# Kernel optimization log

Hardware: AMD Instinct MI355X
Metric: run time of the kernel (lower is better)

The kernel has to match this reference:

```python
import jax, jax.numpy as jnp
import numpy as np

EPS = 1e-6
ENERGY_THRESHOLD = 0.95
LS_INIT = 1e-5


def setup_inputs() -> dict:
    key = jax.random.key(0)
    k_x, k_u, k_s, k_v = jax.random.split(key, 4)
    dim, max_rank = 4096, 16
    x = jax.random.normal(k_x, (4, 2048, dim), dtype=jnp.float32)
    U = jax.random.normal(k_u, (dim, max_rank), dtype=jnp.float32) * 0.02
    S = jax.random.uniform(k_s, (max_rank,), dtype=jnp.float32)
    V = jax.random.normal(k_v, (max_rank, dim), dtype=jnp.float32) * 0.02
    norm_weight = jnp.ones((dim,), dtype=jnp.float32)
    gamma = jnp.full((dim,), LS_INIT, dtype=jnp.float32)
    return {"x": x, "U": U, "S": S, "V": V,
            "norm_weight": norm_weight, "gamma": gamma}


def _rank_mask(S):
    # Effective rank from singular-value energy (non-differentiable decision,
    # matching torch's .item() host sync which detaches it from autograd).
    s_abs = jnp.abs(S)
    cum = jnp.cumsum(s_abs) / jnp.maximum(s_abs.sum(), 1e-8)
    hit = cum >= ENERGY_THRESHOLD
    r = jnp.where(hit.any(), jnp.argmax(hit) + 1, S.shape[0])
    keep = (jnp.arange(S.shape[0]) < r).astype(S.dtype)
    return jax.lax.stop_gradient(keep)


def reference(x, U, S, V, norm_weight, gamma):
    # RMSNorm (computed in fp32, matching x.float() in torch)
    xf = x.astype(jnp.float32)
    x_norm = (xf * jax.lax.rsqrt(jnp.mean(xf * xf, axis=-1, keepdims=True) + EPS)).astype(x.dtype)
    x_norm = x_norm * norm_weight
    # Adaptive-rank low-rank projection: masking columns >= r equals slicing [:r]
    keep = _rank_mask(S)
    h = jnp.einsum('bsd,dr->bsr', x_norm, U)        # [B,S,max_rank]
    h = h * (S * keep)                               # zero out ranks >= r
    h = jnp.einsum('bsr,rd->bsd', h, V)             # [B,S,dim]
    # LayerScale + residual
    return x + h * gamma
```

## Files before the change

kernel.cpp:

```cpp
#include <hip/hip_runtime.h>

#define DIM   4096
#define RANK  16
#define ROWS  4
#define NT    512
#define NWAVE 8

typedef int   int2v  __attribute__((ext_vector_type(2)));
typedef float f32x4v __attribute__((ext_vector_type(4)));

__device__ __forceinline__ float f4get(const float4& v, int j) {
    switch (j) { case 0: return v.x; case 1: return v.y; case 2: return v.z; default: return v.w; }
}

__global__ __launch_bounds__(256) void transpose_U(const float* __restrict__ U,
                                                   float* __restrict__ Ut) {
    const int d = blockIdx.x * 256 + threadIdx.x;
    const float4* U4 = (const float4*)U;
    float4 u0 = U4[(size_t)d * 4 + 0];
    float4 u1 = U4[(size_t)d * 4 + 1];
    float4 u2 = U4[(size_t)d * 4 + 2];
    float4 u3 = U4[(size_t)d * 4 + 3];
    Ut[ 0*DIM + d] = u0.x; Ut[ 1*DIM + d] = u0.y; Ut[ 2*DIM + d] = u0.z; Ut[ 3*DIM + d] = u0.w;
    Ut[ 4*DIM + d] = u1.x; Ut[ 5*DIM + d] = u1.y; Ut[ 6*DIM + d] = u1.z; Ut[ 7*DIM + d] = u1.w;
    Ut[ 8*DIM + d] = u2.x; Ut[ 9*DIM + d] = u2.y; Ut[10*DIM + d] = u2.z; Ut[11*DIM + d] = u2.w;
    Ut[12*DIM + d] = u3.x; Ut[13*DIM + d] = u3.y; Ut[14*DIM + d] = u3.z; Ut[15*DIM + d] = u3.w;
}

__global__ __launch_bounds__(NT, 2) void arl_fused(
    const float* __restrict__ x,  const float* __restrict__ Ut,
    const float* __restrict__ S,  const float* __restrict__ V,
    const float* __restrict__ nw, const float* __restrict__ gamma,
    float* __restrict__ out)
{
    const int t    = threadIdx.x;
    const int w    = t >> 6;
    const int lane = t & 63;
    const int rg   = w & 3;
    const int dh   = w >> 2;
    const size_t row0 = (size_t)blockIdx.x * ROWS;

    const float4* x4   = (const float4*)(x + row0 * DIM);
    float4*       out4 = (float4*)(out + row0 * DIM);
    const float4* Ut4  = (const float4*)Ut;
    const float4* V4   = (const float4*)V;
    const float4* nw4  = (const float4*)nw;
    const float4* g4   = (const float4*)gamma;

    __shared__ __align__(16) float4 x_lds4[ROWS * (DIM/4)];
    __shared__ float s_ssq[NWAVE][ROWS];
    __shared__ float s_hraw[NWAVE][16];
    __shared__ __align__(16) float s_h[ROWS * RANK];

    #pragma unroll
    for (int i = 0; i < 8; ++i) {
        const int idx = i * NT + t;
        f32x4v val = __builtin_nontemporal_load((const f32x4v*)(x4 + idx));
        *(f32x4v*)&x_lds4[idx] = val;
    }
    __syncthreads();

    float v[16];
    #pragma unroll
    for (int i = 0; i < 16; ++i) v[i] = 0.f;
    float ssq[ROWS] = {0.f, 0.f, 0.f, 0.f};

    #pragma unroll 1
    for (int k = 0; k < 8; ++k) {
        const int d4 = dh * 512 + k * 64 + lane;
        const float4 wv = nw4[d4];
        float4 u[4];
        #pragma unroll
        for (int ql = 0; ql < 4; ++ql)
            u[ql] = Ut4[(size_t)(rg * 4 + ql) * (DIM/4) + d4];
        float4 xr[ROWS];
        #pragma unroll
        for (int r = 0; r < ROWS; ++r) xr[r] = x_lds4[r * (DIM/4) + d4];
        #pragma unroll
        for (int j = 0; j < 4; ++j) {
            const float wj = f4get(wv, j);
            float xn[ROWS];
            #pragma unroll
            for (int r = 0; r < ROWS; ++r) {
                const float xj = f4get(xr[r], j);
                ssq[r] = fmaf(xj, xj, ssq[r]);
                xn[r] = xj * wj;
            }
            #pragma unroll
            for (int ql = 0; ql < 4; ++ql) {
                const float uj = f4get(u[ql], j);
                #pragma unroll
                for (int r = 0; r < ROWS; ++r)
                    v[r*4+ql] = fmaf(xn[r], uj, v[r*4+ql]);
            }
        }
    }

    #pragma unroll
    for (int r = 0; r < ROWS; ++r) {
        float s = ssq[r];
        #pragma unroll
        for (int off = 32; off >= 1; off >>= 1) s += __shfl_xor(s, off, 64);
        if (lane == 0) s_ssq[w][r] = s;
    }

    #pragma unroll
    for (int i = 0; i < 8; ++i) {
        int a = __float_as_int(v[2*i]);
        int b = __float_as_int(v[2*i+1]);
        int2v pr = __builtin_amdgcn_permlane32_swap(a, b, false, false);
        v[i] = __int_as_float(pr.x) + __int_as_float(pr.y);
    }
    #pragma unroll
    for (int s = 1; s <= 3; ++s) {
        const int off = 32 >> s;
        const int n   = 8 >> s;
        const bool hi = (lane >> (5 - s)) & 1;
        #pragma unroll
        for (int i = 0; i < n; ++i) {
            float lo = v[2*i], hg = v[2*i+1];
            float slo = __shfl_xor(lo, off, 64);
            float shg = __shfl_xor(hg, off, 64);
            v[i] = hi ? (hg + shg) : (lo + slo);
        }
    }
    v[0] += __shfl_xor(v[0], 2, 64);
    v[0] += __shfl_xor(v[0], 1, 64);
    {
        const int idx = ((lane >> 5) & 1) | (((lane >> 4) & 1) << 1)
                      | (((lane >> 3) & 1) << 2) | (((lane >> 2) & 1) << 3);
        if ((lane & 3) == 0) s_hraw[w][idx] = v[0];
    }
    __syncthreads();

    if (t < 64) {
        const int r = t >> 4, q = t & 15;
        const int qg = q >> 2, ql = q & 3;
        const float hs = s_hraw[qg][r * 4 + ql] + s_hraw[qg + 4][r * 4 + ql];
        const float tot_ssq = s_ssq[0][r] + s_ssq[4][r];
        const float rstd = rsqrtf(tot_ssq * (1.0f / DIM) + 1e-6f);
        float tot = 0.f;
        #pragma unroll
        for (int i = 0; i < RANK; ++i) tot += fabsf(S[i]);
        const float denom = fmaxf(tot, 1e-8f);
        float cum = 0.f, se = 0.f;
        #pragma unroll
        for (int i = 0; i < RANK; ++i) {
            if (i == q) se = ((cum / denom) < 0.95f) ? S[i] : 0.f;
            cum += fabsf(S[i]);
        }
        s_h[t] = hs * se * rstd;
    }
    __syncthreads();

    const float4* s_h4 = (const float4*)s_h;
    #pragma unroll 1
    for (int k = 0; k < 2; ++k) {
        const int c = k * NT + t;
        float4 acc[ROWS];
        #pragma unroll
        for (int r = 0; r < ROWS; ++r) acc[r] = make_float4(0.f, 0.f, 0.f, 0.f);
        #pragma unroll 1
        for (int qg = 0; qg < 4; ++qg) {
            float4 vv[4];
            #pragma unroll
            for (int ql = 0; ql < 4; ++ql)
                vv[ql] = V4[(size_t)(qg*4 + ql) * (DIM/4) + c];
            #pragma unroll
            for (int r = 0; r < ROWS; ++r) {
                const float4 hq = s_h4[r * 4 + qg];
                #pragma unroll
                for (int ql = 0; ql < 4; ++ql) {
                    const float hqq = f4get(hq, ql);
                    acc[r].x = fmaf(hqq, vv[ql].x, acc[r].x);
                    acc[r].y = fmaf(hqq, vv[ql].y, acc[r].y);
                    acc[r].z = fmaf(hqq, vv[ql].z, acc[r].z);
                    acc[r].w = fmaf(hqq, vv[ql].w, acc[r].w);
                }
            }
        }
        const float4 g = g4[c];
        #pragma unroll
        for (int r = 0; r < ROWS; ++r) {
            const float4 xrr = x_lds4[r * (DIM/4) + c];
            float4 o;
            o.x = fmaf(g.x, acc[r].x, xrr.x);
            o.y = fmaf(g.y, acc[r].y, xrr.y);
            o.z = fmaf(g.z, acc[r].z, xrr.z);
            o.w = fmaf(g.w, acc[r].w, xrr.w);
            __builtin_nontemporal_store(*(const f32x4v*)&o,
                                        (f32x4v*)(out4 + (size_t)r * (DIM/4) + c));
        }
    }
}

extern "C" void kernel_launch(void* const* d_in, const int* in_sizes, int n_in,
                              void* d_out, int out_size, void* d_ws, size_t ws_size,
                              hipStream_t stream) {
    (void)in_sizes; (void)n_in; (void)ws_size;
    const float* x  = (const float*)d_in[0];
    const float* U  = (const float*)d_in[1];
    const float* S  = (const float*)d_in[2];
    const float* V  = (const float*)d_in[3];
    const float* nw = (const float*)d_in[4];
    const float* g  = (const float*)d_in[5];
    float* out = (float*)d_out;
    float* Ut  = (float*)d_ws;

    hipLaunchKernelGGL(transpose_U, dim3(DIM / 256), dim3(256), 0, stream, U, Ut);

    const int rows = out_size / DIM;
    const int grid = rows / ROWS;
    hipLaunchKernelGGL(arl_fused, dim3(grid), dim3(NT), 0, stream,
                       x, Ut, S, V, nw, g, out);
}
```

Measured before the change: 88.84 us.

## Drop LDS staging of x, fold norm weight into U, raise occupancy

Removes the 64KB shared-memory staging of the four x rows and reads x directly from global memory in both phases, relying on cache for the second read. Folds norm_weight into the transposed U in the prep kernel, which removes a load and a multiply per element in the main loop. Raises the launch-bounds occupancy hint from 2 to 8 blocks, which the smaller LDS footprint now allows. The risk is that x is re-read from global memory in the epilogue, and that the tighter register budget causes spills.

```diff
diff --git a/kernel.cpp b/kernel.cpp
--- a/kernel.cpp
+++ b/kernel.cpp
@@ -14,24 +14,25 @@
 }
 
 __global__ __launch_bounds__(256) void transpose_U(const float* __restrict__ U,
+                                                   const float* __restrict__ nw,
                                                    float* __restrict__ Ut) {
     const int d = blockIdx.x * 256 + threadIdx.x;
+    const float wv = nw[d];
     const float4* U4 = (const float4*)U;
     float4 u0 = U4[(size_t)d * 4 + 0];
     float4 u1 = U4[(size_t)d * 4 + 1];
     float4 u2 = U4[(size_t)d * 4 + 2];
     float4 u3 = U4[(size_t)d * 4 + 3];
-    Ut[ 0*DIM + d] = u0.x; Ut[ 1*DIM + d] = u0.y; Ut[ 2*DIM + d] = u0.z; Ut[ 3*DIM + d] = u0.w;
-    Ut[ 4*DIM + d] = u1.x; Ut[ 5*DIM + d] = u1.y; Ut[ 6*DIM + d] = u1.z; Ut[ 7*DIM + d] = u1.w;
-    Ut[ 8*DIM + d] = u2.x; Ut[ 9*DIM + d] = u2.y; Ut[10*DIM + d] = u2.z; Ut[11*DIM + d] = u2.w;
-    Ut[12*DIM + d] = u3.x; Ut[13*DIM + d] = u3.y; Ut[14*DIM + d] = u3.z; Ut[15*DIM + d] = u3.w;
-}
-
-__global__ __launch_bounds__(NT, 2) void arl_fused(
+    Ut[ 0*DIM + d] = u0.x*wv; Ut[ 1*DIM + d] = u0.y*wv; Ut[ 2*DIM + d] = u0.z*wv; Ut[ 3*DIM + d] = u0.w*wv;
+    Ut[ 4*DIM + d] = u1.x*wv; Ut[ 5*DIM + d] = u1.y*wv; Ut[ 6*DIM + d] = u1.z*wv; Ut[ 7*DIM + d] = u1.w*wv;
+    Ut[ 8*DIM + d] = u2.x*wv; Ut[ 9*DIM + d] = u2.y*wv; Ut[10*DIM + d] = u2.z*wv; Ut[11*DIM + d] = u2.w*wv;
+    Ut[12*DIM + d] = u3.x*wv; Ut[13*DIM + d] = u3.y*wv; Ut[14*DIM + d] = u3.z*wv; Ut[15*DIM + d] = u3.w*wv;
+}
+
+__global__ __launch_bounds__(NT, 8) void arl_fused(
     const float* __restrict__ x,  const float* __restrict__ Ut,
     const float* __restrict__ S,  const float* __restrict__ V,
-    const float* __restrict__ nw, const float* __restrict__ gamma,
-    float* __restrict__ out)
+    const float* __restrict__ gamma, float* __restrict__ out)
 {
     const int t    = threadIdx.x;
     const int w    = t >> 6;
@@ -44,22 +45,12 @@
     float4*       out4 = (float4*)(out + row0 * DIM);
     const float4* Ut4  = (const float4*)Ut;
     const float4* V4   = (const float4*)V;
-    const float4* nw4  = (const float4*)nw;
     const float4* g4   = (const float4*)gamma;
 
-    __shared__ __align__(16) float4 x_lds4[ROWS * (DIM/4)];
     __shared__ float s_ssq[NWAVE][ROWS];
     __shared__ float s_hraw[NWAVE][16];
     __shared__ __align__(16) float s_h[ROWS * RANK];
 
-    #pragma unroll
-    for (int i = 0; i < 8; ++i) {
-        const int idx = i * NT + t;
-        f32x4v val = __builtin_nontemporal_load((const f32x4v*)(x4 + idx));
-        *(f32x4v*)&x_lds4[idx] = val;
-    }
-    __syncthreads();
-
     float v[16];
     #pragma unroll
     for (int i = 0; i < 16; ++i) v[i] = 0.f;
@@ -68,30 +59,27 @@
     #pragma unroll 1
     for (int k = 0; k < 8; ++k) {
         const int d4 = dh * 512 + k * 64 + lane;
-        const float4 wv = nw4[d4];
         float4 u[4];
         #pragma unroll
         for (int ql = 0; ql < 4; ++ql)
             u[ql] = Ut4[(size_t)(rg * 4 + ql) * (DIM/4) + d4];
         float4 xr[ROWS];
         #pragma unroll
-        for (int r = 0; r < ROWS; ++r) xr[r] = x_lds4[r * (DIM/4) + d4];
+        for (int r = 0; r < ROWS; ++r) xr[r] = x4[(size_t)r * (DIM/4) + d4];
         #pragma unroll
         for (int j = 0; j < 4; ++j) {
-            const float wj = f4get(wv, j);
-            float xn[ROWS];
+            float xj[ROWS];
             #pragma unroll
             for (int r = 0; r < ROWS; ++r) {
-                const float xj = f4get(xr[r], j);
-                ssq[r] = fmaf(xj, xj, ssq[r]);
-                xn[r] = xj * wj;
+                xj[r] = f4get(xr[r], j);
+                ssq[r] = fmaf(xj[r], xj[r], ssq[r]);
             }
             #pragma unroll
             for (int ql = 0; ql < 4; ++ql) {
                 const float uj = f4get(u[ql], j);
                 #pragma unroll
                 for (int r = 0; r < ROWS; ++r)
-                    v[r*4+ql] = fmaf(xn[r], uj, v[r*4+ql]);
+                    v[r*4+ql] = fmaf(xj[r], uj, v[r*4+ql]);
             }
         }
     }
@@ -182,7 +170,7 @@
         const float4 g = g4[c];
         #pragma unroll
         for (int r = 0; r < ROWS; ++r) {
-            const float4 xrr = x_lds4[r * (DIM/4) + c];
+            const float4 xrr = x4[(size_t)r * (DIM/4) + c];
             float4 o;
             o.x = fmaf(g.x, acc[r].x, xrr.x);
             o.y = fmaf(g.y, acc[r].y, xrr.y);
@@ -207,10 +195,10 @@
     float* out = (float*)d_out;
     float* Ut  = (float*)d_ws;
 
-    hipLaunchKernelGGL(transpose_U, dim3(DIM / 256), dim3(256), 0, stream, U, Ut);
+    hipLaunchKernelGGL(transpose_U, dim3(DIM / 256), dim3(256), 0, stream, U, nw, Ut);
 
     const int rows = out_size / DIM;
     const int grid = rows / ROWS;
     hipLaunchKernelGGL(arl_fused, dim3(grid), dim3(NT), 0, stream,
-                       x, Ut, S, V, nw, g, out);
-}
+                       x, Ut, S, V, g, out);
+}
```

Result: slower. 97.36 us (+9.6%).
